# Performance work log

Measured on AMD Instinct MI355X. Metric: run time of the kernel, lower is better.

## Reference

```python
import jax, jax.numpy as jnp
import numpy as np

# Contiguous token segment lengths per group (static, sums to 4096)
LEN_GROUPS = (256, 512, 768, 384, 640, 512, 576, 448)
NUM_GROUPS, D_IN, D_OUT = 8, 512, 512
BATCH = 16


def setup_inputs() -> dict:
    key = jax.random.key(0)
    k1, k2, k3 = jax.random.split(key, 3)
    T = int(sum(LEN_GROUPS))
    x = jax.random.normal(k1, (BATCH, T, D_IN), dtype=jnp.float32)
    # nn.Linear default init: U(-1/sqrt(fan_in), 1/sqrt(fan_in))
    bound = 1.0 / np.sqrt(D_IN)
    W = jax.random.uniform(k2, (NUM_GROUPS, D_OUT, D_IN), jnp.float32, -bound, bound)
    b = jax.random.uniform(k3, (NUM_GROUPS, D_OUT), jnp.float32, -bound, bound)
    return {"x": x, "W": W, "b": b}


def reference(x, W, b):
    # Per-group Linear over contiguous token segments, then concat along tokens.
    # Loop is over a small static group count; segment bounds are Python ints,
    # so slicing is static and jit-compatible.
    outs = []
    start = 0
    for i, L in enumerate(LEN_GROUPS):
        seg = x[:, start:start + L]                     # [B, L, D_in]
        outs.append(jnp.einsum('btd,od->bto', seg, W[i]) + b[i])  # [B, L, D_out]
        start += L
    return jnp.concatenate(outs, axis=1)               # [B, T, D_out]
```

## Files before the change

kernel.cpp:

```cpp
#include <hip/hip_runtime.h>
#include <hip/hip_bf16.h>
#include <cstdint>

#define BATCH 16
#define TTOT  4096
#define DIN   512
#define DOUT  512
#define NG    8
#define NJOB  33
#define NKT   8

typedef float f32x4 __attribute__((ext_vector_type(4)));
typedef short s16x8 __attribute__((ext_vector_type(8)));

__device__ __forceinline__ short f2b(float f) {
    union { __bf16 b; short s; } u; u.b = (__bf16)f; return u.s;
}

__device__ __constant__ short JT0[NJOB] = {
    0,128, 256,384,512,640, 768,896,1024,1152,1280,1408, 1536,1664,1792,
    1920,2048,2176,2304,2432, 2560,2688,2816,2944, 3072,3200,3328,3456,
    3584, 3648, 3712,3840,3968};
__device__ __constant__ char JG[NJOB] = {
    0,0, 1,1,1,1, 2,2,2,2,2,2, 3,3,3, 4,4,4,4,4, 5,5,5,5, 6,6,6,6, 6, 7, 7,7,7};
__device__ __constant__ char JBM[NJOB] = {
    127,127, 127,127,127,127, 127,127,127,127,127,127, 127,127,127,
    127,127,127,127,127, 127,127,127,127, 127,127,127,127, 63, 63, 127,127,127};

__global__ void wconv_kernel(const float* __restrict__ W, ushort* __restrict__ wbf) {
    int gid = blockIdx.x * 256 + threadIdx.x;
    int c = gid >> 10;
    int q = (gid & 1023) << 4;
    int row = q >> 7;
    int bc  = q & 127;
    int kbyte = bc ^ ((row & 7) << 4);
    int kt = c & 7, nt = (c >> 3) & 3, g = c >> 5;
    const float* wp = W + ((size_t)(g * DOUT + nt * 128 + row)) * DIN
                        + kt * 64 + (kbyte >> 1);
    float4 v0 = *reinterpret_cast<const float4*>(wp);
    float4 v1 = *reinterpret_cast<const float4*>(wp + 4);
    s16x8 o;
    o[0]=f2b(v0.x); o[1]=f2b(v0.y); o[2]=f2b(v0.z); o[3]=f2b(v0.w);
    o[4]=f2b(v1.x); o[5]=f2b(v1.y); o[6]=f2b(v1.z); o[7]=f2b(v1.w);
    *reinterpret_cast<s16x8*>((char*)wbf + (size_t)c * 16384 + q) = o;
}

__launch_bounds__(256, 2)
__global__ void gemm_kernel(const float* __restrict__ x,
                            const ushort* __restrict__ wbf,
                            const float* __restrict__ bias,
                            float* __restrict__ out) {
    __shared__ __align__(16) char smem[81920];

    const int tid  = threadIdx.x;
    const int lane = tid & 63;
    const int wv   = tid >> 6;
    const int wm   = wv >> 1;
    const int wn   = wv & 1;
    const int colf = lane & 15;
    const int kg   = lane >> 4;

    const int p    = blockIdx.x;
    const int l    = (p & 7) * 264 + (p >> 3);
    const int nt   = l & 3;
    const int rest = l >> 2;
    const int job  = rest >> 4;
    const int bb   = rest & 15;
    const int t0   = JT0[job];
    const int g    = JG[job];
    const int bmm1 = JBM[job];
    const int n0   = nt << 7;

    const char* bchunk = (const char*)wbf + (size_t)((g * 4 + nt) * 8) * 16384;

    char* abufs = smem;
    char* bring = smem + 32768;

    const int arow_s = (wv << 5) + (lane >> 3);
    const int col8   = (lane & 7) << 3;
    const float* aptr = x + ((size_t)(bb * TTOT + t0 + arow_s)) * DIN + col8;

    float4 stE[4][2], stO[4][2];

#define ISSUE_A(S, KT_) do {                                                \
        _Pragma("unroll")                                                   \
        for (int j_ = 0; j_ < 4; ++j_) {                                    \
            const float* p_ = aptr + (size_t)(j_ * 8) * DIN + ((KT_) << 6); \
            st##S[j_][0] = *(const float4*)(p_);                            \
            st##S[j_][1] = *(const float4*)(p_ + 4);                        \
        }                                                                   \
    } while (0)

#define ISSUE_B(KT_) do {                                                   \
        const char* src_ = bchunk + (size_t)(KT_) * 16384 + tid * 16;       \
        char* dst_ = bring + ((KT_) % 3) * 16384 + tid * 16;                \
        _Pragma("unroll")                                                   \
        for (int i_ = 0; i_ < 4; ++i_) {                                    \
            __builtin_amdgcn_global_load_lds(                               \
                (const __attribute__((address_space(1))) void*)(src_ + i_ * 4096), \
                (__attribute__((address_space(3))) void*)(dst_ + i_ * 4096),\
                16, 0, 0);                                                  \
        }                                                                   \
    } while (0)

#define CVT_WRITE_A(S, KT_) do {                                            \
        char* ab_ = abufs + ((KT_) & 1) * 16384;                            \
        _Pragma("unroll")                                                   \
        for (int j_ = 0; j_ < 4; ++j_) {                                    \
            float4 lo_ = st##S[j_][0], hi_ = st##S[j_][1];                  \
            s16x8 o_;                                                       \
            o_[0]=f2b(lo_.x); o_[1]=f2b(lo_.y); o_[2]=f2b(lo_.z); o_[3]=f2b(lo_.w); \
            o_[4]=f2b(hi_.x); o_[5]=f2b(hi_.y); o_[6]=f2b(hi_.z); o_[7]=f2b(hi_.w); \
            int row_ = arow_s + j_ * 8;                                     \
            int bc_ = (col8 << 1) ^ ((row_ & 7) << 4);                      \
            *(s16x8*)(ab_ + (row_ << 7) + bc_) = o_;                        \
        }                                                                   \
    } while (0)

#define COMPUTE(KT_) do {                                                   \
        const char* ab_ = abufs + ((KT_) & 1) * 16384;                      \
        const char* bb_ = bring + ((KT_) % 3) * 16384;                      \
        _Pragma("unroll")                                                   \
        for (int ks = 0; ks < 2; ++ks) {                                    \
            const int kb = ks * 64 + (kg << 4);                             \
            s16x8 af[4], bf[4];                                             \
            _Pragma("unroll")                                               \
            for (int mi = 0; mi < 4; ++mi) {                                \
                int r_ = wm * 64 + mi * 16 + colf;                          \
                af[mi] = *(const s16x8*)(ab_ + (r_ << 7) + (kb ^ ((r_ & 7) << 4))); \
            }                                                               \
            _Pragma("unroll")                                               \
            for (int ni = 0; ni < 4; ++ni) {                                \
                int r_ = wn * 64 + ni * 16 + colf;                          \
                bf[ni] = *(const s16x8*)(bb_ + (r_ << 7) + (kb ^ ((r_ & 7) << 4))); \
            }                                                               \
            _Pragma("unroll")                                               \
            for (int mi = 0; mi < 4; ++mi)                                  \
                _Pragma("unroll")                                           \
                for (int ni = 0; ni < 4; ++ni)                              \
                    acc[mi][ni] = __builtin_amdgcn_mfma_f32_16x16x32_bf16(  \
                        af[mi], bf[ni], acc[mi][ni], 0, 0, 0);              \
        }                                                                   \
    } while (0)

#define FENCE   asm volatile("" ::: "memory")
#define WAITV12 asm volatile("s_waitcnt vmcnt(12)" ::: "memory")
#define WAITV0  asm volatile("s_waitcnt vmcnt(0)" ::: "memory")
#define WAITL0  asm volatile("s_waitcnt lgkmcnt(0)" ::: "memory")
#define BARRIER do { FENCE; __builtin_amdgcn_s_barrier(); FENCE; } while (0)

    f32x4 acc[4][4];
#pragma unroll
    for (int mi = 0; mi < 4; ++mi)
#pragma unroll
        for (int ni = 0; ni < 4; ++ni)
            acc[mi][ni] = (f32x4){0.f, 0.f, 0.f, 0.f};

    ISSUE_A(E, 0); ISSUE_B(0);
    FENCE;
    ISSUE_A(O, 1); ISSUE_B(1);
    FENCE;
    CVT_WRITE_A(E, 0);
    WAITV12;
    WAITL0;
    BARRIER;

#pragma unroll
    for (int kt = 0; kt < NKT; ++kt) {
        if (kt + 2 < NKT) {
            if (((kt) & 1) == 0) { ISSUE_A(E, kt + 2); } else { ISSUE_A(O, kt + 2); }
            ISSUE_B(kt + 2);
            FENCE;
        }
        COMPUTE(kt);
        if (kt + 1 < NKT) {
            if (((kt + 1) & 1) == 0) { CVT_WRITE_A(E, kt + 1); }
            else                     { CVT_WRITE_A(O, kt + 1); }
            if (kt + 2 < NKT) { WAITV12; }
            else              { WAITV0;  }
            WAITL0;
            BARRIER;
        }
    }
    BARRIER;

    float* cbuf = (float*)smem;
#pragma unroll
    for (int mi = 0; mi < 4; ++mi)
#pragma unroll
        for (int ni = 0; ni < 4; ++ni) {
            int r0 = wm * 64 + mi * 16 + kg * 4;
            int c  = wn * 64 + ni * 16 + colf;
            f32x4 v = acc[mi][ni];
            cbuf[(r0 + 0) * 132 + c] = v[0];
            cbuf[(r0 + 1) * 132 + c] = v[1];
            cbuf[(r0 + 2) * 132 + c] = v[2];
            cbuf[(r0 + 3) * 132 + c] = v[3];
        }
    WAITL0;
    BARRIER;

    const int rr = tid >> 5;
    const int cc = (tid & 31) << 2;
    float4 bv = *reinterpret_cast<const float4*>(bias + (g << 9) + n0 + cc);
#pragma unroll
    for (int it = 0; it < 16; ++it) {
        int row = it * 8 + rr;
        if (row <= bmm1) {
            float4 v = *reinterpret_cast<const float4*>(cbuf + row * 132 + cc);
            float4 o4; o4.x = v.x + bv.x; o4.y = v.y + bv.y;
                       o4.z = v.z + bv.z; o4.w = v.w + bv.w;
            *reinterpret_cast<float4*>(
                out + ((size_t)(bb * TTOT + t0 + row)) * DOUT + n0 + cc) = o4;
        }
    }
#undef ISSUE_A
#undef ISSUE_B
#undef CVT_WRITE_A
#undef COMPUTE
#undef FENCE
#undef WAITV12
#undef WAITV0
#undef WAITL0
#undef BARRIER
}

__launch_bounds__(256)
__global__ void gemm_fallback(const float* __restrict__ x,
                              const float* __restrict__ W,
                              const float* __restrict__ bias,
                              float* __restrict__ out) {
    __shared__ __align__(16) char smem[49152];
    const int tid  = threadIdx.x;
    const int lane = tid & 63;
    const int wid  = tid >> 6;
    const int wm   = wid >> 1;
    const int wn   = wid & 1;
    const int p  = blockIdx.x;
    const int l  = ((p & 7) << 9) + (p >> 3);
    const int mt = l >> 2;
    const int nt = l & 3;
    const int bb = mt >> 6;
    const int t0 = (mt & 63) << 6;
    const int n0 = nt << 7;
    int g = 0;
    if (t0 >= 256)  g++; if (t0 >= 768)  g++; if (t0 >= 1536) g++;
    if (t0 >= 1920) g++; if (t0 >= 2560) g++; if (t0 >= 3072) g++;
    if (t0 >= 3648) g++;
    const int arow = tid >> 2;
    const int acol = (tid & 3) << 4;
    const float* aptr = x + ((size_t)(bb * TTOT + t0 + arow)) * DIN + acol;
    float4 a0, a1, a2, a3;
    float4 bw0[4], bw1[4];
    auto load_global = [&](int k0) {
        a0 = *(const float4*)(aptr + k0);
        a1 = *(const float4*)(aptr + k0 + 4);
        a2 = *(const float4*)(aptr + k0 + 8);
        a3 = *(const float4*)(aptr + k0 + 12);
#pragma unroll
        for (int pp = 0; pp < 4; ++pp) {
            int idx = pp * 256 + tid;
            int row = idx >> 3, seg = idx & 7;
            const float* wp = W + ((size_t)((g << 9) + n0 + row)) * DIN + k0 + (seg << 3);
            bw0[pp] = *(const float4*)(wp);
            bw1[pp] = *(const float4*)(wp + 4);
        }
    };
    auto swz = [](int row, int bc) { return (row << 7) + (bc ^ ((row & 7) << 4)); };
    auto write_lds = [&](int buf) {
        char* ab  = smem + buf * 8192;
        char* bb_ = smem + 16384 + buf * 16384;
        s16x8 w0, w1;
        w0[0]=f2b(a0.x); w0[1]=f2b(a0.y); w0[2]=f2b(a0.z); w0[3]=f2b(a0.w);
        w0[4]=f2b(a1.x); w0[5]=f2b(a1.y); w0[6]=f2b(a1.z); w0[7]=f2b(a1.w);
        w1[0]=f2b(a2.x); w1[1]=f2b(a2.y); w1[2]=f2b(a2.z); w1[3]=f2b(a2.w);
        w1[4]=f2b(a3.x); w1[5]=f2b(a3.y); w1[6]=f2b(a3.z); w1[7]=f2b(a3.w);
        const int abase2 = acol << 1;
        *(s16x8*)(ab + swz(arow, abase2))      = w0;
        *(s16x8*)(ab + swz(arow, abase2 + 16)) = w1;
#pragma unroll
        for (int pp = 0; pp < 4; ++pp) {
            int idx = pp * 256 + tid;
            int row = idx >> 3, seg = idx & 7;
            s16x8 wvv;
            wvv[0]=f2b(bw0[pp].x); wvv[1]=f2b(bw0[pp].y);
            wvv[2]=f2b(bw0[pp].z); wvv[3]=f2b(bw0[pp].w);
            wvv[4]=f2b(bw1[pp].x); wvv[5]=f2b(bw1[pp].y);
            wvv[6]=f2b(bw1[pp].z); wvv[7]=f2b(bw1[pp].w);
            *(s16x8*)(bb_ + swz(row, seg << 4)) = wvv;
        }
    };
    f32x4 acc[2][4];
#pragma unroll
    for (int mi = 0; mi < 2; ++mi)
#pragma unroll
        for (int ni = 0; ni < 4; ++ni) acc[mi][ni] = (f32x4){0.f,0.f,0.f,0.f};
    const int colf = lane & 15;
    const int kgrp = lane >> 4;
    auto compute = [&](int buf) {
        const char* ab  = smem + buf * 8192;
        const char* bb_ = smem + 16384 + buf * 16384;
#pragma unroll
        for (int ks = 0; ks < 2; ++ks) {
            const int kb = ks * 64 + kgrp * 16;
            s16x8 af[2], bf[4];
#pragma unroll
            for (int mi = 0; mi < 2; ++mi)
                af[mi] = *(const s16x8*)(ab + swz(wm * 32 + mi * 16 + colf, kb));
#pragma unroll
            for (int ni = 0; ni < 4; ++ni)
                bf[ni] = *(const s16x8*)(bb_ + swz(wn * 64 + ni * 16 + colf, kb));
#pragma unroll
            for (int mi = 0; mi < 2; ++mi)
#pragma unroll
                for (int ni = 0; ni < 4; ++ni)
                    acc[mi][ni] = __builtin_amdgcn_mfma_f32_16x16x32_bf16(
                        af[mi], bf[ni], acc[mi][ni], 0, 0, 0);
        }
    };
    load_global(0);
    write_lds(0);
    __syncthreads();
    int buf = 0;
#pragma unroll 1
    for (int kt = 0; kt < 8; ++kt) {
        if (kt < 7) load_global((kt + 1) << 6);
        compute(buf);
        if (kt < 7) write_lds(buf ^ 1);
        __syncthreads();
        buf ^= 1;
    }
    float* cbuf = (float*)smem;
#pragma unroll
    for (int ni = 0; ni < 4; ++ni) {
        const int c = wn * 64 + ni * 16 + colf;
#pragma unroll
        for (int mi = 0; mi < 2; ++mi) {
            const int r = wm * 32 + mi * 16 + kgrp * 4;
            f32x4 v = acc[mi][ni];
            cbuf[(r + 0) * 132 + c] = v[0];
            cbuf[(r + 1) * 132 + c] = v[1];
            cbuf[(r + 2) * 132 + c] = v[2];
            cbuf[(r + 3) * 132 + c] = v[3];
        }
    }
    __syncthreads();
    const int rr = tid >> 5;
    const int cc = (tid & 31) << 2;
    const float4 bv = *(const float4*)(bias + (g << 9) + n0 + cc);
#pragma unroll
    for (int it = 0; it < 8; ++it) {
        const int row = it * 8 + rr;
        float4 v = *(const float4*)(cbuf + row * 132 + cc);
        float4 o4; o4.x = v.x + bv.x; o4.y = v.y + bv.y;
                   o4.z = v.z + bv.z; o4.w = v.w + bv.w;
        *(float4*)(out + ((size_t)(bb * TTOT) + t0 + row) * DOUT + n0 + cc) = o4;
    }
}

extern "C" void kernel_launch(void* const* d_in, const int* in_sizes, int n_in,
                              void* d_out, int out_size, void* d_ws, size_t ws_size,
                              hipStream_t stream) {
    const float* x    = (const float*)d_in[0];
    const float* W    = (const float*)d_in[1];
    const float* bias = (const float*)d_in[2];
    float* out = (float*)d_out;

    const size_t wbytes = (size_t)NG * DOUT * DIN * sizeof(ushort);

    if (ws_size >= wbytes) {
        ushort* wbf = (ushort*)d_ws;
        wconv_kernel<<<1024, 256, 0, stream>>>(W, wbf);
        gemm_kernel<<<NJOB * BATCH * 4, 256, 0, stream>>>(x, wbf, bias, out);
    } else {
        gemm_fallback<<<BATCH * 64 * 4, 256, 0, stream>>>(x, W, bias, out);
    }
}
```

Before: 95.62 us.

## Enlarge GEMM tile to 256x256 with 512-thread blocks and double-buffered LDS

Reworks the grouped GEMM from 128x128 tiles with 256 threads to 256x256 tiles with 512 threads (8 waves, each computing 128x64), using 18 row-jobs per batch and clamping rows for partial tiles. The weight pre-conversion layout is changed to 256-row chunks, B is double-buffered instead of triple-buffered, A prefetch depth is reduced to one stage, and s_setprio is raised around MFMA sections. The epilogue is staged through LDS in eight 32-row passes. The aim is more reuse per loaded byte and fewer redundant A reads across N tiles. In exchange it uses 128KB of LDS and 128 accumulator registers per thread, which limits occupancy, and it gives only 576 blocks.

```diff
diff --git a/kernel.cpp b/kernel.cpp
--- a/kernel.cpp
+++ b/kernel.cpp
@@ -7,7 +7,7 @@
 #define DIN   512
 #define DOUT  512
 #define NG    8
-#define NJOB  33
+#define NJB   18
 #define NKT   8
 
 typedef float f32x4 __attribute__((ext_vector_type(4)));
@@ -17,209 +17,209 @@
     union { __bf16 b; short s; } u; u.b = (__bf16)f; return u.s;
 }
 
-__device__ __constant__ short JT0[NJOB] = {
-    0,128, 256,384,512,640, 768,896,1024,1152,1280,1408, 1536,1664,1792,
-    1920,2048,2176,2304,2432, 2560,2688,2816,2944, 3072,3200,3328,3456,
-    3584, 3648, 3712,3840,3968};
-__device__ __constant__ char JG[NJOB] = {
-    0,0, 1,1,1,1, 2,2,2,2,2,2, 3,3,3, 4,4,4,4,4, 5,5,5,5, 6,6,6,6, 6, 7, 7,7,7};
-__device__ __constant__ char JBM[NJOB] = {
-    127,127, 127,127,127,127, 127,127,127,127,127,127, 127,127,127,
-    127,127,127,127,127, 127,127,127,127, 127,127,127,127, 63, 63, 127,127,127};
+__device__ __constant__ short JT0[NJB] = {
+    0,256,512,768,1024,1280,1536,1792,1920,2176,2432,2560,2816,3072,3328,3584,3648,3904};
+__device__ __constant__ char JG[NJB] = {
+    0,1,1,2,2,2,3,3,4,4,4,5,5,6,6,6,7,7};
+__device__ __constant__ short JVR[NJB] = {
+    256,256,256,256,256,256,256,128,256,256,128,256,256,256,256,64,256,192};
 
 __global__ void wconv_kernel(const float* __restrict__ W, ushort* __restrict__ wbf) {
     int gid = blockIdx.x * 256 + threadIdx.x;
-    int c = gid >> 10;
-    int q = (gid & 1023) << 4;
+    int c = gid >> 11;
+    int q = (gid & 2047) << 4;
     int row = q >> 7;
     int bc  = q & 127;
     int kbyte = bc ^ ((row & 7) << 4);
-    int kt = c & 7, nt = (c >> 3) & 3, g = c >> 5;
-    const float* wp = W + ((size_t)(g * DOUT + nt * 128 + row)) * DIN
-                        + kt * 64 + (kbyte >> 1);
+    int kt = c & 7, nt = (c >> 3) & 1, g = c >> 4;
+    const float* wp = W + ((size_t)((g << 9) + (nt << 8) + row) << 9)
+                        + (kt << 6) + (kbyte >> 1);
     float4 v0 = *reinterpret_cast<const float4*>(wp);
     float4 v1 = *reinterpret_cast<const float4*>(wp + 4);
     s16x8 o;
     o[0]=f2b(v0.x); o[1]=f2b(v0.y); o[2]=f2b(v0.z); o[3]=f2b(v0.w);
     o[4]=f2b(v1.x); o[5]=f2b(v1.y); o[6]=f2b(v1.z); o[7]=f2b(v1.w);
-    *reinterpret_cast<s16x8*>((char*)wbf + (size_t)c * 16384 + q) = o;
-}
-
-__launch_bounds__(256, 2)
+    *reinterpret_cast<s16x8*>((char*)wbf + (size_t)c * 32768 + q) = o;
+}
+
+__launch_bounds__(512, 2)
 __global__ void gemm_kernel(const float* __restrict__ x,
                             const ushort* __restrict__ wbf,
                             const float* __restrict__ bias,
                             float* __restrict__ out) {
-    __shared__ __align__(16) char smem[81920];
+    __shared__ __align__(16) char smem[131072];
 
     const int tid  = threadIdx.x;
     const int lane = tid & 63;
     const int wv   = tid >> 6;
-    const int wm   = wv >> 1;
-    const int wn   = wv & 1;
+    const int wm   = wv >> 2;
+    const int wn   = wv & 3;
     const int colf = lane & 15;
     const int kg   = lane >> 4;
 
-    const int p    = blockIdx.x;
-    const int l    = (p & 7) * 264 + (p >> 3);
-    const int nt   = l & 3;
-    const int rest = l >> 2;
-    const int job  = rest >> 4;
-    const int bb   = rest & 15;
-    const int t0   = JT0[job];
-    const int g    = JG[job];
-    const int bmm1 = JBM[job];
-    const int n0   = nt << 7;
-
-    const char* bchunk = (const char*)wbf + (size_t)((g * 4 + nt) * 8) * 16384;
-
-    char* abufs = smem;
-    char* bring = smem + 32768;
-
-    const int arow_s = (wv << 5) + (lane >> 3);
-    const int col8   = (lane & 7) << 3;
-    const float* aptr = x + ((size_t)(bb * TTOT + t0 + arow_s)) * DIN + col8;
-
-    float4 stE[4][2], stO[4][2];
-
-#define ISSUE_A(S, KT_) do {                                                \
+    const int p     = blockIdx.x;
+    const int mjob  = p >> 1;
+    const int nt    = p & 1;
+    const int batch = mjob / NJB;
+    const int j     = mjob - batch * NJB;
+    const int t0    = JT0[j];
+    const int g     = JG[j];
+    const int vr    = JVR[j];
+    const int n0    = nt << 8;
+
+    const char* bchunk = (const char*)wbf + (size_t)(((g << 1) + nt) << 3) * 32768;
+
+    const int r = tid >> 1;
+    const int h = tid & 1;
+    const int re = (r < vr) ? r : (vr - 1);
+    const float* arow_ptr = x + (((size_t)(batch * TTOT + t0 + re)) << 9) + (h << 5);
+
+    float4 st[4][2];
+
+#define ISSUE_A(KT_) do {                                                   \
         _Pragma("unroll")                                                   \
-        for (int j_ = 0; j_ < 4; ++j_) {                                    \
-            const float* p_ = aptr + (size_t)(j_ * 8) * DIN + ((KT_) << 6); \
-            st##S[j_][0] = *(const float4*)(p_);                            \
-            st##S[j_][1] = *(const float4*)(p_ + 4);                        \
+        for (int j4 = 0; j4 < 4; ++j4) {                                    \
+            const float* p_ = arow_ptr + ((KT_) << 6) + (j4 << 3);          \
+            st[j4][0] = *(const float4*)(p_);                               \
+            st[j4][1] = *(const float4*)(p_ + 4);                           \
         }                                                                   \
     } while (0)
 
+#define CVT_WRITE_A(KT_) do {                                               \
+        char* ab_ = smem + ((KT_) & 1) * 32768;                             \
+        _Pragma("unroll")                                                   \
+        for (int j4 = 0; j4 < 4; ++j4) {                                    \
+            float4 lo_ = st[j4][0], hi_ = st[j4][1];                        \
+            s16x8 o_;                                                       \
+            o_[0]=f2b(lo_.x); o_[1]=f2b(lo_.y); o_[2]=f2b(lo_.z); o_[3]=f2b(lo_.w); \
+            o_[4]=f2b(hi_.x); o_[5]=f2b(hi_.y); o_[6]=f2b(hi_.z); o_[7]=f2b(hi_.w); \
+            int bc_ = ((h << 6) + (j4 << 4)) ^ ((r & 7) << 4);              \
+            *(s16x8*)(ab_ + (r << 7) + bc_) = o_;                           \
+        }                                                                   \
+    } while (0)
+
 #define ISSUE_B(KT_) do {                                                   \
-        const char* src_ = bchunk + (size_t)(KT_) * 16384 + tid * 16;       \
-        char* dst_ = bring + ((KT_) % 3) * 16384 + tid * 16;                \
+        const char* src_ = bchunk + (size_t)(KT_) * 32768 + tid * 16;       \
+        char* dst_ = smem + 65536 + ((KT_) & 1) * 32768 + tid * 16;         \
         _Pragma("unroll")                                                   \
         for (int i_ = 0; i_ < 4; ++i_) {                                    \
             __builtin_amdgcn_global_load_lds(                               \
-                (const __attribute__((address_space(1))) void*)(src_ + i_ * 4096), \
-                (__attribute__((address_space(3))) void*)(dst_ + i_ * 4096),\
+                (const __attribute__((address_space(1))) void*)(src_ + i_ * 8192), \
+                (__attribute__((address_space(3))) void*)(dst_ + i_ * 8192),\
                 16, 0, 0);                                                  \
         }                                                                   \
     } while (0)
 
-#define CVT_WRITE_A(S, KT_) do {                                            \
-        char* ab_ = abufs + ((KT_) & 1) * 16384;                            \
-        _Pragma("unroll")                                                   \
-        for (int j_ = 0; j_ < 4; ++j_) {                                    \
-            float4 lo_ = st##S[j_][0], hi_ = st##S[j_][1];                  \
-            s16x8 o_;                                                       \
-            o_[0]=f2b(lo_.x); o_[1]=f2b(lo_.y); o_[2]=f2b(lo_.z); o_[3]=f2b(lo_.w); \
-            o_[4]=f2b(hi_.x); o_[5]=f2b(hi_.y); o_[6]=f2b(hi_.z); o_[7]=f2b(hi_.w); \
-            int row_ = arow_s + j_ * 8;                                     \
-            int bc_ = (col8 << 1) ^ ((row_ & 7) << 4);                      \
-            *(s16x8*)(ab_ + (row_ << 7) + bc_) = o_;                        \
-        }                                                                   \
-    } while (0)
-
 #define COMPUTE(KT_) do {                                                   \
-        const char* ab_ = abufs + ((KT_) & 1) * 16384;                      \
-        const char* bb_ = bring + ((KT_) % 3) * 16384;                      \
+        const char* ab_ = smem + ((KT_) & 1) * 32768;                       \
+        const char* bb_ = smem + 65536 + ((KT_) & 1) * 32768;               \
+        __builtin_amdgcn_s_setprio(1);                                      \
         _Pragma("unroll")                                                   \
         for (int ks = 0; ks < 2; ++ks) {                                    \
             const int kb = ks * 64 + (kg << 4);                             \
-            s16x8 af[4], bf[4];                                             \
+            s16x8 bf[4];                                                    \
             _Pragma("unroll")                                               \
-            for (int mi = 0; mi < 4; ++mi) {                                \
-                int r_ = wm * 64 + mi * 16 + colf;                          \
-                af[mi] = *(const s16x8*)(ab_ + (r_ << 7) + (kb ^ ((r_ & 7) << 4))); \
+            for (int ni = 0; ni < 4; ++ni) {                                \
+                int rr_ = wn * 64 + ni * 16 + colf;                         \
+                bf[ni] = *(const s16x8*)(bb_ + (rr_ << 7) + (kb ^ ((rr_ & 7) << 4))); \
             }                                                               \
             _Pragma("unroll")                                               \
-            for (int ni = 0; ni < 4; ++ni) {                                \
-                int r_ = wn * 64 + ni * 16 + colf;                          \
-                bf[ni] = *(const s16x8*)(bb_ + (r_ << 7) + (kb ^ ((r_ & 7) << 4))); \
-            }                                                               \
-            _Pragma("unroll")                                               \
-            for (int mi = 0; mi < 4; ++mi)                                  \
+            for (int mi = 0; mi < 8; ++mi) {                                \
+                int rr_ = wm * 128 + mi * 16 + colf;                        \
+                s16x8 af = *(const s16x8*)(ab_ + (rr_ << 7) + (kb ^ ((rr_ & 7) << 4))); \
                 _Pragma("unroll")                                           \
                 for (int ni = 0; ni < 4; ++ni)                              \
                     acc[mi][ni] = __builtin_amdgcn_mfma_f32_16x16x32_bf16(  \
-                        af[mi], bf[ni], acc[mi][ni], 0, 0, 0);              \
+                        af, bf[ni], acc[mi][ni], 0, 0, 0);                  \
+            }                                                               \
         }                                                                   \
+        __builtin_amdgcn_s_setprio(0);                                      \
     } while (0)
 
-#define FENCE   asm volatile("" ::: "memory")
-#define WAITV12 asm volatile("s_waitcnt vmcnt(12)" ::: "memory")
-#define WAITV0  asm volatile("s_waitcnt vmcnt(0)" ::: "memory")
-#define WAITL0  asm volatile("s_waitcnt lgkmcnt(0)" ::: "memory")
+#define FENCE  asm volatile("" ::: "memory")
+#define WAITV8 asm volatile("s_waitcnt vmcnt(8)" ::: "memory")
+#define WAITV0 asm volatile("s_waitcnt vmcnt(0)" ::: "memory")
+#define WAITL0 asm volatile("s_waitcnt lgkmcnt(0)" ::: "memory")
 #define BARRIER do { FENCE; __builtin_amdgcn_s_barrier(); FENCE; } while (0)
 
-    f32x4 acc[4][4];
-#pragma unroll
-    for (int mi = 0; mi < 4; ++mi)
+    f32x4 acc[8][4];
+#pragma unroll
+    for (int mi = 0; mi < 8; ++mi)
 #pragma unroll
         for (int ni = 0; ni < 4; ++ni)
             acc[mi][ni] = (f32x4){0.f, 0.f, 0.f, 0.f};
 
-    ISSUE_A(E, 0); ISSUE_B(0);
+    ISSUE_A(0); ISSUE_B(0);
     FENCE;
-    ISSUE_A(O, 1); ISSUE_B(1);
+    CVT_WRITE_A(0);
+    ISSUE_A(1);
     FENCE;
-    CVT_WRITE_A(E, 0);
-    WAITV12;
+    WAITV8;
     WAITL0;
     BARRIER;
 
 #pragma unroll
     for (int kt = 0; kt < NKT; ++kt) {
-        if (kt + 2 < NKT) {
-            if (((kt) & 1) == 0) { ISSUE_A(E, kt + 2); } else { ISSUE_A(O, kt + 2); }
-            ISSUE_B(kt + 2);
-            FENCE;
-        }
+        if (kt + 1 < NKT) { ISSUE_B(kt + 1); FENCE; }
         COMPUTE(kt);
         if (kt + 1 < NKT) {
-            if (((kt + 1) & 1) == 0) { CVT_WRITE_A(E, kt + 1); }
-            else                     { CVT_WRITE_A(O, kt + 1); }
-            if (kt + 2 < NKT) { WAITV12; }
-            else              { WAITV0;  }
+            CVT_WRITE_A(kt + 1);
+            if (kt + 2 < NKT) { ISSUE_A(kt + 2); FENCE; WAITV8; }
+            else              { WAITV0; }
             WAITL0;
             BARRIER;
         }
     }
-    BARRIER;
-
-    float* cbuf = (float*)smem;
-#pragma unroll
-    for (int mi = 0; mi < 4; ++mi)
-#pragma unroll
-        for (int ni = 0; ni < 4; ++ni) {
-            int r0 = wm * 64 + mi * 16 + kg * 4;
-            int c  = wn * 64 + ni * 16 + colf;
-            f32x4 v = acc[mi][ni];
-            cbuf[(r0 + 0) * 132 + c] = v[0];
-            cbuf[(r0 + 1) * 132 + c] = v[1];
-            cbuf[(r0 + 2) * 132 + c] = v[2];
-            cbuf[(r0 + 3) * 132 + c] = v[3];
-        }
+
     WAITL0;
     BARRIER;
 
-    const int rr = tid >> 5;
-    const int cc = (tid & 31) << 2;
-    float4 bv = *reinterpret_cast<const float4*>(bias + (g << 9) + n0 + cc);
-#pragma unroll
-    for (int it = 0; it < 16; ++it) {
-        int row = it * 8 + rr;
-        if (row <= bmm1) {
-            float4 v = *reinterpret_cast<const float4*>(cbuf + row * 132 + cc);
-            float4 o4; o4.x = v.x + bv.x; o4.y = v.y + bv.y;
-                       o4.z = v.z + bv.z; o4.w = v.w + bv.w;
-            *reinterpret_cast<float4*>(
-                out + ((size_t)(bb * TTOT + t0 + row)) * DOUT + n0 + cc) = o4;
-        }
+    float* cbuf = (float*)smem;
+    float4 bv4[4];
+    const int er = tid >> 4;
+    const int ec = (tid & 15) << 2;
+#pragma unroll
+    for (int i = 0; i < 4; ++i)
+        bv4[i] = *(const float4*)(bias + (g << 9) + n0 + ec + (i << 6));
+
+#pragma unroll
+    for (int pp = 0; pp < 8; ++pp) {
+        if ((wv >> 2) == (pp >> 2)) {
+#pragma unroll
+            for (int m = 0; m < 2; ++m) {
+                const int am = (pp & 3) * 2 + m;
+#pragma unroll
+                for (int ni = 0; ni < 4; ++ni) {
+                    const int base = (m * 16 + kg * 4) * 260 + wn * 64 + ni * 16 + colf;
+                    cbuf[base]       = acc[am][ni][0];
+                    cbuf[base + 260] = acc[am][ni][1];
+                    cbuf[base + 520] = acc[am][ni][2];
+                    cbuf[base + 780] = acc[am][ni][3];
+                }
+            }
+        }
+        WAITL0;
+        BARRIER;
+        const int row = pp * 32 + er;
+        if (row < vr) {
+            float* orow = out + (((size_t)(batch * TTOT + t0 + row)) << 9) + n0;
+#pragma unroll
+            for (int i = 0; i < 4; ++i) {
+                float4 v = *(const float4*)(cbuf + er * 260 + ec + (i << 6));
+                float4 o4;
+                o4.x = v.x + bv4[i].x; o4.y = v.y + bv4[i].y;
+                o4.z = v.z + bv4[i].z; o4.w = v.w + bv4[i].w;
+                *(float4*)(orow + ec + (i << 6)) = o4;
+            }
+        }
+        BARRIER;
     }
 #undef ISSUE_A
+#undef CVT_WRITE_A
 #undef ISSUE_B
-#undef CVT_WRITE_A
 #undef COMPUTE
 #undef FENCE
-#undef WAITV12
+#undef WAITV8
 #undef WAITV0
 #undef WAITL0
 #undef BARRIER
@@ -266,7 +266,7 @@
             bw1[pp] = *(const float4*)(wp + 4);
         }
     };
-    auto swz = [](int row, int bc) { return (row << 7) + (bc ^ ((row & 7) << 4)); };
+    auto swzf = [](int row, int bc) { return (row << 7) + (bc ^ ((row & 7) << 4)); };
     auto write_lds = [&](int buf) {
         char* ab  = smem + buf * 8192;
         char* bb_ = smem + 16384 + buf * 16384;
@@ -276,8 +276,8 @@
         w1[0]=f2b(a2.x); w1[1]=f2b(a2.y); w1[2]=f2b(a2.z); w1[3]=f2b(a2.w);
         w1[4]=f2b(a3.x); w1[5]=f2b(a3.y); w1[6]=f2b(a3.z); w1[7]=f2b(a3.w);
         const int abase2 = acol << 1;
-        *(s16x8*)(ab + swz(arow, abase2))      = w0;
-        *(s16x8*)(ab + swz(arow, abase2 + 16)) = w1;
+        *(s16x8*)(ab + swzf(arow, abase2))      = w0;
+        *(s16x8*)(ab + swzf(arow, abase2 + 16)) = w1;
 #pragma unroll
         for (int pp = 0; pp < 4; ++pp) {
             int idx = pp * 256 + tid;
@@ -287,7 +287,7 @@
             wvv[2]=f2b(bw0[pp].z); wvv[3]=f2b(bw0[pp].w);
             wvv[4]=f2b(bw1[pp].x); wvv[5]=f2b(bw1[pp].y);
             wvv[6]=f2b(bw1[pp].z); wvv[7]=f2b(bw1[pp].w);
-            *(s16x8*)(bb_ + swz(row, seg << 4)) = wvv;
+            *(s16x8*)(bb_ + swzf(row, seg << 4)) = wvv;
         }
     };
     f32x4 acc[2][4];
@@ -306,10 +306,10 @@
             s16x8 af[2], bf[4];
 #pragma unroll
             for (int mi = 0; mi < 2; ++mi)
-                af[mi] = *(const s16x8*)(ab + swz(wm * 32 + mi * 16 + colf, kb));
+                af[mi] = *(const s16x8*)(ab + swzf(wm * 32 + mi * 16 + colf, kb));
 #pragma unroll
             for (int ni = 0; ni < 4; ++ni)
-                bf[ni] = *(const s16x8*)(bb_ + swz(wn * 64 + ni * 16 + colf, kb));
+                bf[ni] = *(const s16x8*)(bb_ + swzf(wn * 64 + ni * 16 + colf, kb));
 #pragma unroll
             for (int mi = 0; mi < 2; ++mi)
 #pragma unroll
@@ -347,13 +347,13 @@
     __syncthreads();
     const int rr = tid >> 5;
     const int cc = (tid & 31) << 2;
-    const float4 bv = *(const float4*)(bias + (g << 9) + n0 + cc);
+    const float4 bvv = *(const float4*)(bias + (g << 9) + n0 + cc);
 #pragma unroll
     for (int it = 0; it < 8; ++it) {
         const int row = it * 8 + rr;
         float4 v = *(const float4*)(cbuf + row * 132 + cc);
-        float4 o4; o4.x = v.x + bv.x; o4.y = v.y + bv.y;
-                   o4.z = v.z + bv.z; o4.w = v.w + bv.w;
+        float4 o4; o4.x = v.x + bvv.x; o4.y = v.y + bvv.y;
+                   o4.z = v.z + bvv.z; o4.w = v.w + bvv.w;
         *(float4*)(out + ((size_t)(bb * TTOT) + t0 + row) * DOUT + n0 + cc) = o4;
     }
 }
@@ -371,7 +371,7 @@
     if (ws_size >= wbytes) {
         ushort* wbf = (ushort*)d_ws;
         wconv_kernel<<<1024, 256, 0, stream>>>(W, wbf);
-        gemm_kernel<<<NJOB * BATCH * 4, 256, 0, stream>>>(x, wbf, bias, out);
+        gemm_kernel<<<NJB * BATCH * 2, 512, 0, stream>>>(x, wbf, bias, out);
     } else {
         gemm_fallback<<<BATCH * 64 * 4, 256, 0, stream>>>(x, W, bias, out);
     }
```

New measurement: 115.2 us. 20.5% more time.

## Retile grouped GEMM to 64x512 blocks with full-N B staging

Applied to the files above, without the earlier changes.

Each block now computes a 64-row by 512-column output tile with 512 threads. Every wave owns 64 output columns, so each fp32 activation tile is loaded and converted to bf16 once instead of once per 128-column slice. Because every segment length is a multiple of 64, tiles map directly to groups without partial-tile masking. The weight pre-conversion is reorganized into 64KB full-N chunks, and the B staging drops from a triple-buffered to a double-buffered ring. The cost is about 144KB of shared memory per block, which limits CU occupancy, and a shallower prefetch pipeline.

```diff
diff --git a/kernel.cpp b/kernel.cpp
--- a/kernel.cpp
+++ b/kernel.cpp
@@ -7,7 +7,6 @@
 #define DIN   512
 #define DOUT  512
 #define NG    8
-#define NJOB  33
 #define NKT   8
 
 typedef float f32x4 __attribute__((ext_vector_type(4)));
@@ -17,121 +16,103 @@
     union { __bf16 b; short s; } u; u.b = (__bf16)f; return u.s;
 }
 
-__device__ __constant__ short JT0[NJOB] = {
-    0,128, 256,384,512,640, 768,896,1024,1152,1280,1408, 1536,1664,1792,
-    1920,2048,2176,2304,2432, 2560,2688,2816,2944, 3072,3200,3328,3456,
-    3584, 3648, 3712,3840,3968};
-__device__ __constant__ char JG[NJOB] = {
-    0,0, 1,1,1,1, 2,2,2,2,2,2, 3,3,3, 4,4,4,4,4, 5,5,5,5, 6,6,6,6, 6, 7, 7,7,7};
-__device__ __constant__ char JBM[NJOB] = {
-    127,127, 127,127,127,127, 127,127,127,127,127,127, 127,127,127,
-    127,127,127,127,127, 127,127,127,127, 127,127,127,127, 63, 63, 127,127,127};
-
 __global__ void wconv_kernel(const float* __restrict__ W, ushort* __restrict__ wbf) {
     int gid = blockIdx.x * 256 + threadIdx.x;
-    int c = gid >> 10;
-    int q = (gid & 1023) << 4;
+    int c = gid >> 12;
+    int q = (gid & 4095) << 4;
     int row = q >> 7;
     int bc  = q & 127;
-    int kbyte = bc ^ ((row & 7) << 4);
-    int kt = c & 7, nt = (c >> 3) & 3, g = c >> 5;
-    const float* wp = W + ((size_t)(g * DOUT + nt * 128 + row)) * DIN
-                        + kt * 64 + (kbyte >> 1);
+    int k = ((c & 7) << 6) + ((bc ^ ((row & 7) << 4)) >> 1);
+    int g = c >> 3;
+    const float* wp = W + ((size_t)((g << 9) + row) << 9) + k;
     float4 v0 = *reinterpret_cast<const float4*>(wp);
     float4 v1 = *reinterpret_cast<const float4*>(wp + 4);
     s16x8 o;
     o[0]=f2b(v0.x); o[1]=f2b(v0.y); o[2]=f2b(v0.z); o[3]=f2b(v0.w);
     o[4]=f2b(v1.x); o[5]=f2b(v1.y); o[6]=f2b(v1.z); o[7]=f2b(v1.w);
-    *reinterpret_cast<s16x8*>((char*)wbf + (size_t)c * 16384 + q) = o;
-}
-
-__launch_bounds__(256, 2)
+    *reinterpret_cast<s16x8*>((char*)wbf + (size_t)c * 65536 + q) = o;
+}
+
+__launch_bounds__(512, 2)
 __global__ void gemm_kernel(const float* __restrict__ x,
                             const ushort* __restrict__ wbf,
                             const float* __restrict__ bias,
                             float* __restrict__ out) {
-    __shared__ __align__(16) char smem[81920];
+    __shared__ __align__(16) char smem[147456];
 
     const int tid  = threadIdx.x;
     const int lane = tid & 63;
     const int wv   = tid >> 6;
-    const int wm   = wv >> 1;
-    const int wn   = wv & 1;
     const int colf = lane & 15;
     const int kg   = lane >> 4;
 
-    const int p    = blockIdx.x;
-    const int l    = (p & 7) * 264 + (p >> 3);
-    const int nt   = l & 3;
-    const int rest = l >> 2;
-    const int job  = rest >> 4;
-    const int bb   = rest & 15;
-    const int t0   = JT0[job];
-    const int g    = JG[job];
-    const int bmm1 = JBM[job];
-    const int n0   = nt << 7;
-
-    const char* bchunk = (const char*)wbf + (size_t)((g * 4 + nt) * 8) * 16384;
-
-    char* abufs = smem;
-    char* bring = smem + 32768;
-
-    const int arow_s = (wv << 5) + (lane >> 3);
-    const int col8   = (lane & 7) << 3;
-    const float* aptr = x + ((size_t)(bb * TTOT + t0 + arow_s)) * DIN + col8;
-
-    float4 stE[4][2], stO[4][2];
+    const int p  = blockIdx.x;
+    const int l  = ((p & 7) << 7) + (p >> 3);
+    const int mt = l >> 4;
+    const int batch = l & 15;
+    const int t0 = mt << 6;
+    int g = 0;
+    if (mt >= 4)  g++; if (mt >= 12) g++; if (mt >= 24) g++;
+    if (mt >= 30) g++; if (mt >= 40) g++; if (mt >= 48) g++;
+    if (mt >= 57) g++;
+
+    const char* bchunk = (const char*)wbf + (size_t)(g << 3) * 65536;
+
+    const int arow = tid >> 3;
+    const int koff = ((tid & 7) ^ (arow & 7)) << 3;
+    const float* aptr = x + ((size_t)((batch << 12) + t0 + arow) << 9) + koff;
+    const int awb = (arow << 7) + ((tid & 7) << 4);
+
+    float4 aE[2], aO[2];
+    f32x4 acc[4][4];
+#pragma unroll
+    for (int mi = 0; mi < 4; ++mi)
+#pragma unroll
+        for (int ni = 0; ni < 4; ++ni)
+            acc[mi][ni] = (f32x4){0.f, 0.f, 0.f, 0.f};
 
 #define ISSUE_A(S, KT_) do {                                                \
+        const float* p_ = aptr + ((KT_) << 6);                              \
+        a##S[0] = *(const float4*)(p_);                                     \
+        a##S[1] = *(const float4*)(p_ + 4);                                 \
+    } while (0)
+
+#define CVT_WRITE_A(S, KT_) do {                                            \
+        s16x8 o_;                                                           \
+        o_[0]=f2b(a##S[0].x); o_[1]=f2b(a##S[0].y);                         \
+        o_[2]=f2b(a##S[0].z); o_[3]=f2b(a##S[0].w);                         \
+        o_[4]=f2b(a##S[1].x); o_[5]=f2b(a##S[1].y);                         \
+        o_[6]=f2b(a##S[1].z); o_[7]=f2b(a##S[1].w);                         \
+        *(s16x8*)(smem + (((KT_) & 1) << 13) + awb) = o_;                   \
+    } while (0)
+
+#define ISSUE_B(KT_) do {                                                   \
+        const char* s_ = bchunk + ((size_t)(KT_) << 16) + tid * 16;         \
+        char* d_ = smem + 16384 + (((KT_) & 1) << 16) + tid * 16;           \
         _Pragma("unroll")                                                   \
-        for (int j_ = 0; j_ < 4; ++j_) {                                    \
-            const float* p_ = aptr + (size_t)(j_ * 8) * DIN + ((KT_) << 6); \
-            st##S[j_][0] = *(const float4*)(p_);                            \
-            st##S[j_][1] = *(const float4*)(p_ + 4);                        \
-        }                                                                   \
-    } while (0)
-
-#define ISSUE_B(KT_) do {                                                   \
-        const char* src_ = bchunk + (size_t)(KT_) * 16384 + tid * 16;       \
-        char* dst_ = bring + ((KT_) % 3) * 16384 + tid * 16;                \
-        _Pragma("unroll")                                                   \
-        for (int i_ = 0; i_ < 4; ++i_) {                                    \
+        for (int i_ = 0; i_ < 8; ++i_) {                                    \
             __builtin_amdgcn_global_load_lds(                               \
-                (const __attribute__((address_space(1))) void*)(src_ + i_ * 4096), \
-                (__attribute__((address_space(3))) void*)(dst_ + i_ * 4096),\
+                (const __attribute__((address_space(1))) void*)(s_ + i_ * 8192), \
+                (__attribute__((address_space(3))) void*)(d_ + i_ * 8192),  \
                 16, 0, 0);                                                  \
         }                                                                   \
     } while (0)
 
-#define CVT_WRITE_A(S, KT_) do {                                            \
-        char* ab_ = abufs + ((KT_) & 1) * 16384;                            \
-        _Pragma("unroll")                                                   \
-        for (int j_ = 0; j_ < 4; ++j_) {                                    \
-            float4 lo_ = st##S[j_][0], hi_ = st##S[j_][1];                  \
-            s16x8 o_;                                                       \
-            o_[0]=f2b(lo_.x); o_[1]=f2b(lo_.y); o_[2]=f2b(lo_.z); o_[3]=f2b(lo_.w); \
-            o_[4]=f2b(hi_.x); o_[5]=f2b(hi_.y); o_[6]=f2b(hi_.z); o_[7]=f2b(hi_.w); \
-            int row_ = arow_s + j_ * 8;                                     \
-            int bc_ = (col8 << 1) ^ ((row_ & 7) << 4);                      \
-            *(s16x8*)(ab_ + (row_ << 7) + bc_) = o_;                        \
-        }                                                                   \
-    } while (0)
-
 #define COMPUTE(KT_) do {                                                   \
-        const char* ab_ = abufs + ((KT_) & 1) * 16384;                      \
-        const char* bb_ = bring + ((KT_) % 3) * 16384;                      \
+        const char* ab_ = smem + (((KT_) & 1) << 13);                       \
+        const char* bb_ = smem + 16384 + (((KT_) & 1) << 16);               \
         _Pragma("unroll")                                                   \
         for (int ks = 0; ks < 2; ++ks) {                                    \
             const int kb = ks * 64 + (kg << 4);                             \
             s16x8 af[4], bf[4];                                             \
             _Pragma("unroll")                                               \
             for (int mi = 0; mi < 4; ++mi) {                                \
-                int r_ = wm * 64 + mi * 16 + colf;                          \
+                int r_ = mi * 16 + colf;                                    \
                 af[mi] = *(const s16x8*)(ab_ + (r_ << 7) + (kb ^ ((r_ & 7) << 4))); \
             }                                                               \
             _Pragma("unroll")                                               \
             for (int ni = 0; ni < 4; ++ni) {                                \
-                int r_ = wn * 64 + ni * 16 + colf;                          \
+                int r_ = (wv << 6) + ni * 16 + colf;                        \
                 bf[ni] = *(const s16x8*)(bb_ + (r_ << 7) + (kb ^ ((r_ & 7) << 4))); \
             }                                                               \
             _Pragma("unroll")                                               \
@@ -143,86 +124,82 @@
         }                                                                   \
     } while (0)
 
-#define FENCE   asm volatile("" ::: "memory")
-#define WAITV12 asm volatile("s_waitcnt vmcnt(12)" ::: "memory")
-#define WAITV0  asm volatile("s_waitcnt vmcnt(0)" ::: "memory")
-#define WAITL0  asm volatile("s_waitcnt lgkmcnt(0)" ::: "memory")
-#define BARRIER do { FENCE; __builtin_amdgcn_s_barrier(); FENCE; } while (0)
-
-    f32x4 acc[4][4];
-#pragma unroll
-    for (int mi = 0; mi < 4; ++mi)
-#pragma unroll
-        for (int ni = 0; ni < 4; ++ni)
-            acc[mi][ni] = (f32x4){0.f, 0.f, 0.f, 0.f};
-
-    ISSUE_A(E, 0); ISSUE_B(0);
+#define FENCE  asm volatile("" ::: "memory")
+#define WAITV2 asm volatile("s_waitcnt vmcnt(2)" ::: "memory")
+#define WAITV0 asm volatile("s_waitcnt vmcnt(0)" ::: "memory")
+#define WAITL0 asm volatile("s_waitcnt lgkmcnt(0)" ::: "memory")
+#define BAR    __builtin_amdgcn_s_barrier()
+
+    ISSUE_A(E, 0);
     FENCE;
-    ISSUE_A(O, 1); ISSUE_B(1);
+    ISSUE_B(0);
+    FENCE;
+    ISSUE_A(O, 1);
     FENCE;
     CVT_WRITE_A(E, 0);
-    WAITV12;
+    WAITV2;
     WAITL0;
-    BARRIER;
+    BAR;
 
 #pragma unroll
     for (int kt = 0; kt < NKT; ++kt) {
+        if (kt + 1 < NKT) { ISSUE_B(kt + 1); FENCE; }
         if (kt + 2 < NKT) {
-            if (((kt) & 1) == 0) { ISSUE_A(E, kt + 2); } else { ISSUE_A(O, kt + 2); }
-            ISSUE_B(kt + 2);
+            if (((kt + 2) & 1) == 0) { ISSUE_A(E, kt + 2); }
+            else                     { ISSUE_A(O, kt + 2); }
             FENCE;
         }
         COMPUTE(kt);
         if (kt + 1 < NKT) {
             if (((kt + 1) & 1) == 0) { CVT_WRITE_A(E, kt + 1); }
             else                     { CVT_WRITE_A(O, kt + 1); }
-            if (kt + 2 < NKT) { WAITV12; }
-            else              { WAITV0;  }
+            if (kt + 2 < NKT) { WAITV2; }
+            else              { WAITV0; }
             WAITL0;
-            BARRIER;
-        }
-    }
-    BARRIER;
+            BAR;
+        }
+    }
+    BAR;
 
     float* cbuf = (float*)smem;
 #pragma unroll
     for (int mi = 0; mi < 4; ++mi)
 #pragma unroll
         for (int ni = 0; ni < 4; ++ni) {
-            int r0 = wm * 64 + mi * 16 + kg * 4;
-            int c  = wn * 64 + ni * 16 + colf;
+            const int r0 = mi * 16 + kg * 4;
+            const int c  = (wv << 6) + ni * 16 + colf;
             f32x4 v = acc[mi][ni];
-            cbuf[(r0 + 0) * 132 + c] = v[0];
-            cbuf[(r0 + 1) * 132 + c] = v[1];
-            cbuf[(r0 + 2) * 132 + c] = v[2];
-            cbuf[(r0 + 3) * 132 + c] = v[3];
+            cbuf[(r0 + 0) * 516 + c] = v[0];
+            cbuf[(r0 + 1) * 516 + c] = v[1];
+            cbuf[(r0 + 2) * 516 + c] = v[2];
+            cbuf[(r0 + 3) * 516 + c] = v[3];
         }
     WAITL0;
-    BARRIER;
-
-    const int rr = tid >> 5;
-    const int cc = (tid & 31) << 2;
-    float4 bv = *reinterpret_cast<const float4*>(bias + (g << 9) + n0 + cc);
-#pragma unroll
-    for (int it = 0; it < 16; ++it) {
-        int row = it * 8 + rr;
-        if (row <= bmm1) {
-            float4 v = *reinterpret_cast<const float4*>(cbuf + row * 132 + cc);
-            float4 o4; o4.x = v.x + bv.x; o4.y = v.y + bv.y;
-                       o4.z = v.z + bv.z; o4.w = v.w + bv.w;
-            *reinterpret_cast<float4*>(
-                out + ((size_t)(bb * TTOT + t0 + row)) * DOUT + n0 + cc) = o4;
-        }
+    BAR;
+
+    const int rr = tid >> 3;
+    const int c0 = (tid & 7) << 6;
+    float* orow = out + ((size_t)((batch << 12) + t0 + rr) << 9) + c0;
+    const float* crow = cbuf + rr * 516 + c0;
+    const float* brow = bias + (g << 9) + c0;
+#pragma unroll
+    for (int i = 0; i < 16; ++i) {
+        float4 v  = *(const float4*)(crow + (i << 2));
+        float4 bv = *(const float4*)(brow + (i << 2));
+        float4 o4;
+        o4.x = v.x + bv.x; o4.y = v.y + bv.y;
+        o4.z = v.z + bv.z; o4.w = v.w + bv.w;
+        *(float4*)(orow + (i << 2)) = o4;
     }
 #undef ISSUE_A
+#undef CVT_WRITE_A
 #undef ISSUE_B
-#undef CVT_WRITE_A
 #undef COMPUTE
 #undef FENCE
-#undef WAITV12
+#undef WAITV2
 #undef WAITV0
 #undef WAITL0
-#undef BARRIER
+#undef BAR
 }
 
 __launch_bounds__(256)
@@ -266,7 +243,7 @@
             bw1[pp] = *(const float4*)(wp + 4);
         }
     };
-    auto swz = [](int row, int bc) { return (row << 7) + (bc ^ ((row & 7) << 4)); };
+    auto swzf = [](int row, int bc) { return (row << 7) + (bc ^ ((row & 7) << 4)); };
     auto write_lds = [&](int buf) {
         char* ab  = smem + buf * 8192;
         char* bb_ = smem + 16384 + buf * 16384;
@@ -276,8 +253,8 @@
         w1[0]=f2b(a2.x); w1[1]=f2b(a2.y); w1[2]=f2b(a2.z); w1[3]=f2b(a2.w);
         w1[4]=f2b(a3.x); w1[5]=f2b(a3.y); w1[6]=f2b(a3.z); w1[7]=f2b(a3.w);
         const int abase2 = acol << 1;
-        *(s16x8*)(ab + swz(arow, abase2))      = w0;
-        *(s16x8*)(ab + swz(arow, abase2 + 16)) = w1;
+        *(s16x8*)(ab + swzf(arow, abase2))      = w0;
+        *(s16x8*)(ab + swzf(arow, abase2 + 16)) = w1;
 #pragma unroll
         for (int pp = 0; pp < 4; ++pp) {
             int idx = pp * 256 + tid;
@@ -287,7 +264,7 @@
             wvv[2]=f2b(bw0[pp].z); wvv[3]=f2b(bw0[pp].w);
             wvv[4]=f2b(bw1[pp].x); wvv[5]=f2b(bw1[pp].y);
             wvv[6]=f2b(bw1[pp].z); wvv[7]=f2b(bw1[pp].w);
-            *(s16x8*)(bb_ + swz(row, seg << 4)) = wvv;
+            *(s16x8*)(bb_ + swzf(row, seg << 4)) = wvv;
         }
     };
     f32x4 acc[2][4];
@@ -306,10 +283,10 @@
             s16x8 af[2], bf[4];
 #pragma unroll
             for (int mi = 0; mi < 2; ++mi)
-                af[mi] = *(const s16x8*)(ab + swz(wm * 32 + mi * 16 + colf, kb));
+                af[mi] = *(const s16x8*)(ab + swzf(wm * 32 + mi * 16 + colf, kb));
 #pragma unroll
             for (int ni = 0; ni < 4; ++ni)
-                bf[ni] = *(const s16x8*)(bb_ + swz(wn * 64 + ni * 16 + colf, kb));
+                bf[ni] = *(const s16x8*)(bb_ + swzf(wn * 64 + ni * 16 + colf, kb));
 #pragma unroll
             for (int mi = 0; mi < 2; ++mi)
 #pragma unroll
@@ -336,24 +313,24 @@
         const int c = wn * 64 + ni * 16 + colf;
 #pragma unroll
         for (int mi = 0; mi < 2; ++mi) {
-            const int r = wm * 32 + mi * 16 + kgrp * 4;
+            const int rr2 = wm * 32 + mi * 16 + kgrp * 4;
             f32x4 v = acc[mi][ni];
-            cbuf[(r + 0) * 132 + c] = v[0];
-            cbuf[(r + 1) * 132 + c] = v[1];
-            cbuf[(r + 2) * 132 + c] = v[2];
-            cbuf[(r + 3) * 132 + c] = v[3];
+            cbuf[(rr2 + 0) * 132 + c] = v[0];
+            cbuf[(rr2 + 1) * 132 + c] = v[1];
+            cbuf[(rr2 + 2) * 132 + c] = v[2];
+            cbuf[(rr2 + 3) * 132 + c] = v[3];
         }
     }
     __syncthreads();
     const int rr = tid >> 5;
     const int cc = (tid & 31) << 2;
-    const float4 bv = *(const float4*)(bias + (g << 9) + n0 + cc);
+    const float4 bvv = *(const float4*)(bias + (g << 9) + n0 + cc);
 #pragma unroll
     for (int it = 0; it < 8; ++it) {
         const int row = it * 8 + rr;
         float4 v = *(const float4*)(cbuf + row * 132 + cc);
-        float4 o4; o4.x = v.x + bv.x; o4.y = v.y + bv.y;
-                   o4.z = v.z + bv.z; o4.w = v.w + bv.w;
+        float4 o4; o4.x = v.x + bvv.x; o4.y = v.y + bvv.y;
+                   o4.z = v.z + bvv.z; o4.w = v.w + bvv.w;
         *(float4*)(out + ((size_t)(bb * TTOT) + t0 + row) * DOUT + n0 + cc) = o4;
     }
 }
@@ -371,7 +348,7 @@
     if (ws_size >= wbytes) {
         ushort* wbf = (ushort*)d_ws;
         wconv_kernel<<<1024, 256, 0, stream>>>(W, wbf);
-        gemm_kernel<<<NJOB * BATCH * 4, 256, 0, stream>>>(x, wbf, bias, out);
+        gemm_kernel<<<1024, 512, 0, stream>>>(x, wbf, bias, out);
     } else {
         gemm_fallback<<<BATCH * 64 * 4, 256, 0, stream>>>(x, W, bias, out);
     }
```

Result: slower. 116.5 us (+21.9%).
